# Optimization experiments

Measured on AMD Instinct MI355X. Metric: run time of the kernel, lower is better.

## Reference

```python
import jax, jax.numpy as jnp
import numpy as np

N = 50000      # nodes
E = 800000     # edges (no self loops; added in reference like PyG add_self_loops)
IN = 128       # in_channel
C = 64         # out_channel
K = 64         # cos_num (correlation embedding dim)
H = 1          # heads
NEG_SLOPE = 0.2


def setup_inputs() -> dict:
    key = jax.random.key(0)
    ks = jax.random.split(key, 10)
    x = jax.random.normal(ks[0], (N, IN), dtype=jnp.float32)
    corrs = jax.random.normal(ks[1], (N, K), dtype=jnp.float32)
    # random edges guaranteed to have src != dst (original remove_self_loops)
    src = jax.random.randint(ks[2], (E,), 0, N)
    off = jax.random.randint(ks[3], (E,), 1, N)
    dst = (src + off) % N
    edge_index = jnp.stack([src, dst]).astype(jnp.int32)  # [2, E]
    W = jax.random.normal(ks[4], (IN, H * C), dtype=jnp.float32) / np.sqrt(IN)
    att_i = jax.random.normal(ks[5], (1, H, C), dtype=jnp.float32) * 0.1
    att_j = jax.random.normal(ks[6], (1, H, C), dtype=jnp.float32) * 0.1
    att_em_i = jax.random.normal(ks[7], (1, H, K), dtype=jnp.float32) * 0.1
    att_em_j = jax.random.normal(ks[8], (1, H, K), dtype=jnp.float32) * 0.1
    bias = jnp.zeros((C,), dtype=jnp.float32)
    return {"x": x, "edge_index": edge_index, "corrs": corrs, "W": W,
            "att_i": att_i, "att_j": att_j,
            "att_em_i": att_em_i, "att_em_j": att_em_j, "bias": bias}


def reference(x, edge_index, corrs, W, att_i, att_j, att_em_i, att_em_j, bias):
    # add self loops (original: remove_self_loops then add_self_loops)
    loops = jnp.arange(N, dtype=edge_index.dtype)
    src = jnp.concatenate([edge_index[0], loops])   # [E+N] message sources (x_j)
    dst = jnp.concatenate([edge_index[1], loops])   # [E+N] message targets (x_i)

    g = (x @ W).reshape(N, H, C)                    # linear projection, [N,H,C]
    gj = g[src]                                     # source features per edge [E+N,H,C]
    gi = g[dst]                                     # target features per edge
    ej = corrs[src][:, None, :]                     # [E+N,1,K] broadcast over heads
    ei = corrs[dst][:, None, :]

    # GAT-style score on concatenated key [g || corr]
    alpha = (jnp.sum(gi * att_i, -1) + jnp.sum(ei * att_em_i, -1)
             + jnp.sum(gj * att_j, -1) + jnp.sum(ej * att_em_j, -1))   # [E+N,H]
    alpha = jax.nn.leaky_relu(alpha, NEG_SLOPE)

    # neighbor softmax over incoming edges of each target node (per head)
    amax = jax.ops.segment_max(alpha, dst, num_segments=N)
    ex = jnp.exp(alpha - amax[dst])
    denom = jax.ops.segment_sum(ex, dst, num_segments=N)
    a = ex / (denom[dst] + 1e-16)                   # [E+N,H]

    # scatter-add weighted messages
    out = jax.ops.segment_sum(gj * a[..., None], dst, num_segments=N)  # [N,H,C]
    out = out.mean(axis=1) + bias                    # concat=False -> head mean

    # wrapper: float cast + ReLU
    return jax.nn.relu(out.astype(jnp.float32))
```

## Files before the change

kernel.cpp:

```cpp
#include <hip/hip_runtime.h>
#include <hip/hip_bf16.h>
#include <math.h>

#define IN_DIM 128
#define C_DIM 64

typedef short bf16x8 __attribute__((ext_vector_type(8)));
typedef float f32x4 __attribute__((ext_vector_type(4)));

static __device__ __forceinline__ unsigned short f2bf(float f) {
    unsigned int u = __float_as_uint(f);
    u += 0x7FFFu + ((u >> 16) & 1u);
    return (unsigned short)(u >> 16);
}
static __device__ __forceinline__ float bf2f(unsigned short h) {
    return __uint_as_float(((unsigned int)h) << 16);
}

#define BKT_CHUNK 4096

__global__ __launch_bounds__(256) void k_gemm_bucket(
    const float* __restrict__ x, const float* __restrict__ W,
    const float* __restrict__ corrs,
    const float* __restrict__ att_i, const float* __restrict__ att_j,
    const float* __restrict__ att_em_i, const float* __restrict__ att_em_j,
    unsigned short* __restrict__ g_bf, float* __restrict__ s_i, float* __restrict__ s_j,
    int N, int GB,
    const int* __restrict__ src, const int* __restrict__ dst,
    int E, int NB, int CAP,
    int* __restrict__ bucket_cnt, unsigned int* __restrict__ staging)
{
    __shared__ __attribute__((aligned(16))) unsigned short WT[2][64][128];
    __shared__ int cnt[128];
    __shared__ int run[128];
    __shared__ int cur[128];

    int tid = threadIdx.x;

    if (blockIdx.x >= GB) {
        if (tid < 128) cnt[tid] = 0;
        __syncthreads();

        int T = E + N;
        int base = (blockIdx.x - GB) * BKT_CHUNK;
#pragma unroll
        for (int k = 0; k < BKT_CHUNK / 256; ++k) {
            int i = base + k * 256 + tid;
            if (i < T) {
                int d = (i < E) ? dst[i] : (i - E);
                atomicAdd(&cnt[d >> 9], 1);
            }
        }
        __syncthreads();
        if (tid < NB && cnt[tid] > 0) run[tid] = atomicAdd(&bucket_cnt[tid], cnt[tid]);
        if (tid < 128) cur[tid] = 0;
        __syncthreads();
#pragma unroll
        for (int k = 0; k < BKT_CHUNK / 256; ++k) {
            int i = base + k * 256 + tid;
            if (i < T) {
                int d, s;
                if (i < E) { d = dst[i]; s = src[i]; }
                else       { d = i - E; s = d; }
                int b = d >> 9;
                int ofs = atomicAdd(&cur[b], 1);
                int pos = run[b] + ofs;
                if (pos < CAP)
                    staging[(size_t)b * CAP + pos] =
                        (unsigned)s | ((unsigned)(d & 511) << 16);
            }
        }
        return;
    }

#pragma unroll
    for (int p = 0; p < 8; ++p) {
        int f = p * 1024 + tid * 4;
        f32x4 w4 = *(const f32x4*)(W + f);
        int k  = f >> 6;
        int c0 = f & 63;
#pragma unroll
        for (int i = 0; i < 4; ++i) {
            int c = c0 + i;
            float wv = w4[i];
            unsigned short hi = f2bf(wv);
            unsigned short lo = f2bf(wv - bf2f(hi));
            int ks = k ^ ((c & 7) << 3);
            WT[0][c][ks] = hi;
            WT[1][c][ks] = lo;
        }
    }
    __syncthreads();

    int wv = tid >> 6, lane = tid & 63;
    int mrow = lane & 15;
    int kgrp = lane >> 4;
    int row  = blockIdx.x * 64 + wv * 16 + mrow;
    int rowc = min(row, N - 1);

    f32x4 acc[4];
#pragma unroll
    for (int t = 0; t < 4; ++t) { f32x4 z = {0.f, 0.f, 0.f, 0.f}; acc[t] = z; }

    f32x4 xa[4], xb[4];
#pragma unroll
    for (int s = 0; s < 4; ++s) {
        const float* xp = x + (size_t)rowc * IN_DIM + s * 32 + kgrp * 8;
        xa[s] = *(const f32x4*)xp;
        xb[s] = *(const f32x4*)(xp + 4);
    }

#pragma unroll
    for (int s = 0; s < 4; ++s) {
        bf16x8 ah, al;
#pragma unroll
        for (int i = 0; i < 4; ++i) {
            unsigned short h0 = f2bf(xa[s][i]);
            ah[i]     = (short)h0;
            al[i]     = (short)f2bf(xa[s][i] - bf2f(h0));
            unsigned short h1 = f2bf(xb[s][i]);
            ah[4 + i] = (short)h1;
            al[4 + i] = (short)f2bf(xb[s][i] - bf2f(h1));
        }
        int kbase = s * 32 + kgrp * 8;
#pragma unroll
        for (int t = 0; t < 4; ++t) {
            int c  = t * 16 + mrow;
            int ks = kbase ^ ((c & 7) << 3);
            bf16x8 bh = *(const bf16x8*)&WT[0][c][ks];
            bf16x8 bl = *(const bf16x8*)&WT[1][c][ks];
            acc[t] = __builtin_amdgcn_mfma_f32_16x16x32_bf16(ah, bh, acc[t], 0, 0, 0);
            acc[t] = __builtin_amdgcn_mfma_f32_16x16x32_bf16(ah, bl, acc[t], 0, 0, 0);
            acc[t] = __builtin_amdgcn_mfma_f32_16x16x32_bf16(al, bh, acc[t], 0, 0, 0);
        }
    }

    float ai[4], aj[4], aei[4], aej[4];
#pragma unroll
    for (int t = 0; t < 4; ++t) {
        ai[t]  = att_i[t * 16 + mrow];
        aj[t]  = att_j[t * 16 + mrow];
        aei[t] = att_em_i[t * 16 + mrow];
        aej[t] = att_em_j[t * 16 + mrow];
    }
    int crow_base = blockIdx.x * 64 + wv * 16 + (lane >> 4) * 4;
#pragma unroll
    for (int r = 0; r < 4; ++r) {
        int grow  = crow_base + r;
        int growc = min(grow, N - 1);
        float vi = 0.f, vj = 0.f;
        ushort4 hv;
#pragma unroll
        for (int t = 0; t < 4; ++t) {
            float gv = acc[t][r];
            float cv = corrs[(size_t)growc * 64 + t * 16 + mrow];
            unsigned short h = f2bf(gv);
            if (t == 0) hv.x = h; else if (t == 1) hv.y = h;
            else if (t == 2) hv.z = h; else hv.w = h;
            vi = fmaf(gv, ai[t], fmaf(cv, aei[t], vi));
            vj = fmaf(gv, aj[t], fmaf(cv, aej[t], vj));
        }
        if (grow < N)
            *(ushort4*)(g_bf + (size_t)grow * C_DIM + mrow * 4) = hv;
#pragma unroll
        for (int o = 1; o < 16; o <<= 1) {
            vi += __shfl_xor(vi, o);
            vj += __shfl_xor(vj, o);
        }
        if (mrow == 0 && grow < N) { s_i[grow] = vi; s_j[grow] = vj; }
    }
}

__global__ __launch_bounds__(256) void k_scatter(
    const unsigned int* __restrict__ staging, const int* __restrict__ bucket_cnt,
    int N, int CAP,
    const float* __restrict__ s_i, const float* __restrict__ s_j,
    int* __restrict__ row_start, int* __restrict__ row_end,
    unsigned int* __restrict__ edge_rec)
{
    __shared__ int cnt[512];
    __shared__ int off[513];
    __shared__ int cur[512];
    __shared__ int wsum[4];
    __shared__ float si_l[512];

    int b = blockIdx.x, t = threadIdx.x;
    int lo = b << 9;
    int hi = min(lo + 512, N);
    int bcnt = min(bucket_cnt[b], CAP);
    const unsigned int* sb = staging + (size_t)b * CAP;

    cnt[2 * t] = 0; cnt[2 * t + 1] = 0;
    if (lo + 2 * t     < N) si_l[2 * t]     = s_i[lo + 2 * t];
    if (lo + 2 * t + 1 < N) si_l[2 * t + 1] = s_i[lo + 2 * t + 1];
    __syncthreads();

    for (int r = t; r < bcnt; r += 256)
        atomicAdd(&cnt[(sb[r] >> 16) & 511], 1);
    __syncthreads();

    int a0 = cnt[2 * t], a1 = cnt[2 * t + 1];
    int s = a0 + a1;
    int lane = t & 63, wv = t >> 6;
    int incl = s;
#pragma unroll
    for (int o = 1; o < 64; o <<= 1) {
        int u = __shfl_up(incl, o);
        if (lane >= o) incl += u;
    }
    if (lane == 63) wsum[wv] = incl;
    __syncthreads();
    int woff = 0;
    for (int w = 0; w < wv; ++w) woff += wsum[w];
    int ex = woff + incl - s;
    off[2 * t] = ex;       off[2 * t + 1] = ex + a0;
    cur[2 * t] = ex;       cur[2 * t + 1] = ex + a0;
    if (t == 255) off[512] = woff + incl;
    __syncthreads();

    int rawb = b * CAP;
    for (int i = t; i < hi - lo; i += 256) {
        row_start[lo + i] = rawb + off[i];
        row_end[lo + i]   = rawb + off[i + 1];
    }
    for (int r = t; r < bcnt; r += 256) {
        unsigned int rec = sb[r];
        int dl   = (rec >> 16) & 511;
        int srcn = rec & 0xFFFFu;
        float a = si_l[dl] + s_j[srcn];
        a = (a > 0.f) ? a : 0.2f * a;
        float w = __expf(a);
        int slot = atomicAdd(&cur[dl], 1);
        edge_rec[rawb + slot] = ((unsigned)f2bf(w) << 16) | (unsigned)srcn;
    }
}

__global__ __launch_bounds__(256) void k_aggregate(
    const unsigned short* __restrict__ g_bf,
    const int* __restrict__ row_start, const int* __restrict__ row_end,
    const unsigned int* __restrict__ edge_rec,
    const float* __restrict__ bias, float* __restrict__ out, int N)
{
    int wave = threadIdx.x >> 6, lane = threadIdx.x & 63;
    int n = blockIdx.x * 4 + wave;
    if (n >= N) return;

    int start = row_start[n];
    int end   = row_end[n];

    int grp = lane >> 3;
    int cl  = lane & 7;
    float a0 = 0.f, a1 = 0.f, a2 = 0.f, a3 = 0.f;
    float a4 = 0.f, a5 = 0.f, a6 = 0.f, a7 = 0.f, den = 0.f;
#pragma unroll 2
    for (int e0 = start; e0 < end; e0 += 8) {
        int e = e0 + grp;
        if (e < end) {
            unsigned int rec = edge_rec[e];
            int   srcn = rec & 0xFFFFu;
            float w    = bf2f((unsigned short)(rec >> 16));
            const ushort4* gp = (const ushort4*)(g_bf + (size_t)srcn * C_DIM + (cl << 3));
            ushort4 g0 = gp[0];
            ushort4 g1 = gp[1];
            a0 = fmaf(w, bf2f(g0.x), a0);
            a1 = fmaf(w, bf2f(g0.y), a1);
            a2 = fmaf(w, bf2f(g0.z), a2);
            a3 = fmaf(w, bf2f(g0.w), a3);
            a4 = fmaf(w, bf2f(g1.x), a4);
            a5 = fmaf(w, bf2f(g1.y), a5);
            a6 = fmaf(w, bf2f(g1.z), a6);
            a7 = fmaf(w, bf2f(g1.w), a7);
            den += w;
        }
    }
#pragma unroll
    for (int o = 8; o < 64; o <<= 1) {
        a0  += __shfl_xor(a0, o);
        a1  += __shfl_xor(a1, o);
        a2  += __shfl_xor(a2, o);
        a3  += __shfl_xor(a3, o);
        a4  += __shfl_xor(a4, o);
        a5  += __shfl_xor(a5, o);
        a6  += __shfl_xor(a6, o);
        a7  += __shfl_xor(a7, o);
        den += __shfl_xor(den, o);
    }
    if (grp == 0) {
        float inv = 1.f / (den + 1e-16f);
        float av[8] = {a0, a1, a2, a3, a4, a5, a6, a7};
        float* op = out + (size_t)n * C_DIM;
#pragma unroll
        for (int j = 0; j < 8; ++j) {
            int p  = (cl << 3) + j;
            int ch = ((p & 3) << 4) + (p >> 2);
            op[ch] = fmaxf(fmaf(av[j], inv, bias[ch]), 0.f);
        }
    }
}

extern "C" void kernel_launch(void* const* d_in, const int* in_sizes, int n_in,
                              void* d_out, int out_size, void* d_ws, size_t ws_size,
                              hipStream_t stream)
{
    const float* x        = (const float*)d_in[0];
    const int*   eidx     = (const int*)  d_in[1];
    const float* corrs    = (const float*)d_in[2];
    const float* W        = (const float*)d_in[3];
    const float* att_i    = (const float*)d_in[4];
    const float* att_j    = (const float*)d_in[5];
    const float* att_em_i = (const float*)d_in[6];
    const float* att_em_j = (const float*)d_in[7];
    const float* bias     = (const float*)d_in[8];
    float* out = (float*)d_out;

    int N = in_sizes[0] / IN_DIM;
    int E = in_sizes[1] / 2;
    const int* src = eidx;
    const int* dst = eidx + E;

    int T  = E + N;
    int NB = (N + 511) >> 9;
    int CAP = ((T + NB - 1) / NB);
    CAP = CAP + CAP / 4;
    CAP = (CAP + 63) & ~63;

    char* ws = (char*)d_ws;
    size_t off = 0;
    auto alloc = [&](size_t bytes) -> void* {
        void* p = ws + off;
        off += (bytes + 255) & ~(size_t)255;
        return p;
    };
    unsigned short* g_bf = (unsigned short*)alloc((size_t)N * C_DIM * sizeof(unsigned short));
    float* s_i       = (float*)alloc((size_t)N * sizeof(float));
    float* s_j       = (float*)alloc((size_t)N * sizeof(float));
    unsigned int* staging  = (unsigned int*)alloc((size_t)NB * CAP * sizeof(unsigned int));
    unsigned int* edge_rec = (unsigned int*)alloc((size_t)NB * CAP * sizeof(unsigned int));
    int*   row_start = (int*)alloc((size_t)N * sizeof(int));
    int*   row_end   = (int*)alloc((size_t)N * sizeof(int));
    int*   bucket_cnt= (int*)alloc(128 * sizeof(int));
    (void)ws_size; (void)n_in; (void)out_size;

    hipMemsetAsync(bucket_cnt, 0, 128 * sizeof(int), stream);

    int GB = (N + 63) / 64;
    int BB = (T + BKT_CHUNK - 1) / BKT_CHUNK;
    k_gemm_bucket<<<GB + BB, 256, 0, stream>>>(
        x, W, corrs, att_i, att_j, att_em_i, att_em_j, g_bf, s_i, s_j,
        N, GB, src, dst, E, NB, CAP, bucket_cnt, staging);

    k_scatter<<<NB, 256, 0, stream>>>(
        staging, bucket_cnt, N, CAP, s_i, s_j, row_start, row_end, edge_rec);

    k_aggregate<<<(N + 3) / 4, 256, 0, stream>>>(
        g_bf, row_start, row_end, edge_rec, bias, out, N);
}
```

Measured before the change: 86.29 us.

## Fuse GEMM/bucket, scatter and aggregate into one cooperative persistent kernel

Merges the three kernels into a single cooperative kernel that uses grid-wide syncs between phases, with blocks striding over virtual block indices and shared memory overlaid through a union. The goal is to remove two kernel-launch gaps and the tail effects between phases. In exchange it adds grid.sync costs and caps the grid at occupancy times 256 CUs. The scatter phase now runs on only NB (~98) blocks while the rest of the grid waits, and the occupancy query plus cooperative launch add host-side overhead.

```diff
diff --git a/kernel.cpp b/kernel.cpp
--- a/kernel.cpp
+++ b/kernel.cpp
@@ -1,9 +1,13 @@
 #include <hip/hip_runtime.h>
+#include <hip/hip_cooperative_groups.h>
 #include <hip/hip_bf16.h>
 #include <math.h>
 
+namespace cg = cooperative_groups;
+
 #define IN_DIM 128
 #define C_DIM 64
+#define BKT_CHUNK 4096
 
 typedef short bf16x8 __attribute__((ext_vector_type(8)));
 typedef float f32x4 __attribute__((ext_vector_type(4)));
@@ -17,283 +21,278 @@
     return __uint_as_float(((unsigned int)h) << 16);
 }
 
-#define BKT_CHUNK 4096
-
-__global__ __launch_bounds__(256) void k_gemm_bucket(
+struct SmemG { unsigned short WT[2][64][128]; };
+struct SmemB { int cnt[128]; int run[128]; int cur[128]; };
+struct SmemS { int cnt[512]; int off[513]; int cur[512];
+               int wsum[4]; float si_l[512]; };
+union  SmemU { SmemG g; SmemB b; SmemS s; };
+
+__global__ __launch_bounds__(256) void k_fused(
     const float* __restrict__ x, const float* __restrict__ W,
     const float* __restrict__ corrs,
     const float* __restrict__ att_i, const float* __restrict__ att_j,
     const float* __restrict__ att_em_i, const float* __restrict__ att_em_j,
     unsigned short* __restrict__ g_bf, float* __restrict__ s_i, float* __restrict__ s_j,
-    int N, int GB,
     const int* __restrict__ src, const int* __restrict__ dst,
-    int E, int NB, int CAP,
-    int* __restrict__ bucket_cnt, unsigned int* __restrict__ staging)
+    int N, int E, int GB, int BB, int NB, int CAP,
+    int* __restrict__ bucket_cnt, unsigned int* __restrict__ staging,
+    unsigned int* __restrict__ edge_rec,
+    int* __restrict__ row_start, int* __restrict__ row_end,
+    const float* __restrict__ bias, float* __restrict__ out)
 {
-    __shared__ __attribute__((aligned(16))) unsigned short WT[2][64][128];
-    __shared__ int cnt[128];
-    __shared__ int run[128];
-    __shared__ int cur[128];
-
+    __shared__ SmemU sm;
+    cg::grid_group grid = cg::this_grid();
     int tid = threadIdx.x;
-
-    if (blockIdx.x >= GB) {
-        if (tid < 128) cnt[tid] = 0;
-        __syncthreads();
-
-        int T = E + N;
-        int base = (blockIdx.x - GB) * BKT_CHUNK;
-#pragma unroll
-        for (int k = 0; k < BKT_CHUNK / 256; ++k) {
-            int i = base + k * 256 + tid;
-            if (i < T) {
-                int d = (i < E) ? dst[i] : (i - E);
-                atomicAdd(&cnt[d >> 9], 1);
-            }
-        }
-        __syncthreads();
-        if (tid < NB && cnt[tid] > 0) run[tid] = atomicAdd(&bucket_cnt[tid], cnt[tid]);
-        if (tid < 128) cur[tid] = 0;
-        __syncthreads();
-#pragma unroll
-        for (int k = 0; k < BKT_CHUNK / 256; ++k) {
-            int i = base + k * 256 + tid;
-            if (i < T) {
-                int d, s;
-                if (i < E) { d = dst[i]; s = src[i]; }
-                else       { d = i - E; s = d; }
-                int b = d >> 9;
-                int ofs = atomicAdd(&cur[b], 1);
-                int pos = run[b] + ofs;
-                if (pos < CAP)
-                    staging[(size_t)b * CAP + pos] =
-                        (unsigned)s | ((unsigned)(d & 511) << 16);
-            }
-        }
-        return;
+    int T = E + N;
+
+    for (int vb = blockIdx.x; vb < GB + BB; vb += gridDim.x) {
+        if (vb >= GB) {
+            if (tid < 128) sm.b.cnt[tid] = 0;
+            __syncthreads();
+            int base = (vb - GB) * BKT_CHUNK;
+#pragma unroll
+            for (int k = 0; k < BKT_CHUNK / 256; ++k) {
+                int i = base + k * 256 + tid;
+                if (i < T) {
+                    int d = (i < E) ? dst[i] : (i - E);
+                    atomicAdd(&sm.b.cnt[d >> 9], 1);
+                }
+            }
+            __syncthreads();
+            if (tid < NB && sm.b.cnt[tid] > 0)
+                sm.b.run[tid] = atomicAdd(&bucket_cnt[tid], sm.b.cnt[tid]);
+            if (tid < 128) sm.b.cur[tid] = 0;
+            __syncthreads();
+#pragma unroll
+            for (int k = 0; k < BKT_CHUNK / 256; ++k) {
+                int i = base + k * 256 + tid;
+                if (i < T) {
+                    int d, s;
+                    if (i < E) { d = dst[i]; s = src[i]; }
+                    else       { d = i - E; s = d; }
+                    int b = d >> 9;
+                    int ofs = atomicAdd(&sm.b.cur[b], 1);
+                    int pos = sm.b.run[b] + ofs;
+                    if (pos < CAP)
+                        staging[(size_t)b * CAP + pos] =
+                            (unsigned)s | ((unsigned)(d & 511) << 16);
+                }
+            }
+        } else {
+#pragma unroll
+            for (int p = 0; p < 8; ++p) {
+                int f = p * 1024 + tid * 4;
+                f32x4 w4 = *(const f32x4*)(W + f);
+                int k  = f >> 6;
+                int c0 = f & 63;
+#pragma unroll
+                for (int i = 0; i < 4; ++i) {
+                    int c = c0 + i;
+                    float wv2 = w4[i];
+                    unsigned short hi = f2bf(wv2);
+                    unsigned short lo = f2bf(wv2 - bf2f(hi));
+                    int ks = k ^ ((c & 7) << 3);
+                    sm.g.WT[0][c][ks] = hi;
+                    sm.g.WT[1][c][ks] = lo;
+                }
+            }
+            __syncthreads();
+
+            int wv = tid >> 6, lane = tid & 63;
+            int mrow = lane & 15;
+            int kgrp = lane >> 4;
+            int row  = vb * 64 + wv * 16 + mrow;
+            int rowc = min(row, N - 1);
+
+            f32x4 acc[4];
+#pragma unroll
+            for (int t = 0; t < 4; ++t) { f32x4 z = {0.f, 0.f, 0.f, 0.f}; acc[t] = z; }
+
+            f32x4 xa[4], xb[4];
+#pragma unroll
+            for (int s = 0; s < 4; ++s) {
+                const float* xp = x + (size_t)rowc * IN_DIM + s * 32 + kgrp * 8;
+                xa[s] = *(const f32x4*)xp;
+                xb[s] = *(const f32x4*)(xp + 4);
+            }
+
+#pragma unroll
+            for (int s = 0; s < 4; ++s) {
+                bf16x8 ah, al;
+#pragma unroll
+                for (int i = 0; i < 4; ++i) {
+                    unsigned short h0 = f2bf(xa[s][i]);
+                    ah[i]     = (short)h0;
+                    al[i]     = (short)f2bf(xa[s][i] - bf2f(h0));
+                    unsigned short h1 = f2bf(xb[s][i]);
+                    ah[4 + i] = (short)h1;
+                    al[4 + i] = (short)f2bf(xb[s][i] - bf2f(h1));
+                }
+                int kbase = s * 32 + kgrp * 8;
+#pragma unroll
+                for (int t = 0; t < 4; ++t) {
+                    int c  = t * 16 + mrow;
+                    int ks = kbase ^ ((c & 7) << 3);
+                    bf16x8 bh = *(const bf16x8*)&sm.g.WT[0][c][ks];
+                    bf16x8 bl = *(const bf16x8*)&sm.g.WT[1][c][ks];
+                    acc[t] = __builtin_amdgcn_mfma_f32_16x16x32_bf16(ah, bh, acc[t], 0, 0, 0);
+                    acc[t] = __builtin_amdgcn_mfma_f32_16x16x32_bf16(ah, bl, acc[t], 0, 0, 0);
+                    acc[t] = __builtin_amdgcn_mfma_f32_16x16x32_bf16(al, bh, acc[t], 0, 0, 0);
+                }
+            }
+
+            float ai[4], aj[4], aei[4], aej[4];
+#pragma unroll
+            for (int t = 0; t < 4; ++t) {
+                ai[t]  = att_i[t * 16 + mrow];
+                aj[t]  = att_j[t * 16 + mrow];
+                aei[t] = att_em_i[t * 16 + mrow];
+                aej[t] = att_em_j[t * 16 + mrow];
+            }
+            int crow_base = vb * 64 + wv * 16 + (lane >> 4) * 4;
+#pragma unroll
+            for (int r = 0; r < 4; ++r) {
+                int grow  = crow_base + r;
+                int growc = min(grow, N - 1);
+                float vi = 0.f, vj = 0.f;
+                ushort4 hv;
+#pragma unroll
+                for (int t = 0; t < 4; ++t) {
+                    float gv = acc[t][r];
+                    float cv = corrs[(size_t)growc * 64 + t * 16 + mrow];
+                    unsigned short h = f2bf(gv);
+                    if (t == 0) hv.x = h; else if (t == 1) hv.y = h;
+                    else if (t == 2) hv.z = h; else hv.w = h;
+                    vi = fmaf(gv, ai[t], fmaf(cv, aei[t], vi));
+                    vj = fmaf(gv, aj[t], fmaf(cv, aej[t], vj));
+                }
+                if (grow < N)
+                    *(ushort4*)(g_bf + (size_t)grow * C_DIM + mrow * 4) = hv;
+#pragma unroll
+                for (int o = 1; o < 16; o <<= 1) {
+                    vi += __shfl_xor(vi, o);
+                    vj += __shfl_xor(vj, o);
+                }
+                if (mrow == 0 && grow < N) { s_i[grow] = vi; s_j[grow] = vj; }
+            }
+        }
+        __syncthreads();
     }
 
-#pragma unroll
-    for (int p = 0; p < 8; ++p) {
-        int f = p * 1024 + tid * 4;
-        f32x4 w4 = *(const f32x4*)(W + f);
-        int k  = f >> 6;
-        int c0 = f & 63;
-#pragma unroll
-        for (int i = 0; i < 4; ++i) {
-            int c = c0 + i;
-            float wv = w4[i];
-            unsigned short hi = f2bf(wv);
-            unsigned short lo = f2bf(wv - bf2f(hi));
-            int ks = k ^ ((c & 7) << 3);
-            WT[0][c][ks] = hi;
-            WT[1][c][ks] = lo;
-        }
+    grid.sync();
+
+    for (int b = blockIdx.x; b < NB; b += gridDim.x) {
+        int t = tid;
+        int lo = b << 9;
+        int hi = min(lo + 512, N);
+        int bcnt = min(bucket_cnt[b], CAP);
+        const unsigned int* sb = staging + (size_t)b * CAP;
+
+        sm.s.cnt[2 * t] = 0; sm.s.cnt[2 * t + 1] = 0;
+        if (lo + 2 * t     < N) sm.s.si_l[2 * t]     = s_i[lo + 2 * t];
+        if (lo + 2 * t + 1 < N) sm.s.si_l[2 * t + 1] = s_i[lo + 2 * t + 1];
+        __syncthreads();
+
+        for (int r = t; r < bcnt; r += 256)
+            atomicAdd(&sm.s.cnt[(sb[r] >> 16) & 511], 1);
+        __syncthreads();
+
+        int a0 = sm.s.cnt[2 * t], a1 = sm.s.cnt[2 * t + 1];
+        int s = a0 + a1;
+        int lane = t & 63, wv = t >> 6;
+        int incl = s;
+#pragma unroll
+        for (int o = 1; o < 64; o <<= 1) {
+            int u = __shfl_up(incl, o);
+            if (lane >= o) incl += u;
+        }
+        if (lane == 63) sm.s.wsum[wv] = incl;
+        __syncthreads();
+        int woff = 0;
+        for (int w = 0; w < wv; ++w) woff += sm.s.wsum[w];
+        int ex = woff + incl - s;
+        sm.s.off[2 * t] = ex;       sm.s.off[2 * t + 1] = ex + a0;
+        sm.s.cur[2 * t] = ex;       sm.s.cur[2 * t + 1] = ex + a0;
+        if (t == 255) sm.s.off[512] = woff + incl;
+        __syncthreads();
+
+        int rawb = b * CAP;
+        for (int i = t; i < hi - lo; i += 256) {
+            row_start[lo + i] = rawb + sm.s.off[i];
+            row_end[lo + i]   = rawb + sm.s.off[i + 1];
+        }
+        for (int r = t; r < bcnt; r += 256) {
+            unsigned int rec = sb[r];
+            int dl   = (rec >> 16) & 511;
+            int srcn = rec & 0xFFFFu;
+            float a = sm.s.si_l[dl] + s_j[srcn];
+            a = (a > 0.f) ? a : 0.2f * a;
+            float w = __expf(a);
+            int slot = atomicAdd(&sm.s.cur[dl], 1);
+            edge_rec[rawb + slot] = ((unsigned)f2bf(w) << 16) | (unsigned)srcn;
+        }
+        __syncthreads();
     }
-    __syncthreads();
-
-    int wv = tid >> 6, lane = tid & 63;
-    int mrow = lane & 15;
-    int kgrp = lane >> 4;
-    int row  = blockIdx.x * 64 + wv * 16 + mrow;
-    int rowc = min(row, N - 1);
-
-    f32x4 acc[4];
-#pragma unroll
-    for (int t = 0; t < 4; ++t) { f32x4 z = {0.f, 0.f, 0.f, 0.f}; acc[t] = z; }
-
-    f32x4 xa[4], xb[4];
-#pragma unroll
-    for (int s = 0; s < 4; ++s) {
-        const float* xp = x + (size_t)rowc * IN_DIM + s * 32 + kgrp * 8;
-        xa[s] = *(const f32x4*)xp;
-        xb[s] = *(const f32x4*)(xp + 4);
-    }
-
-#pragma unroll
-    for (int s = 0; s < 4; ++s) {
-        bf16x8 ah, al;
-#pragma unroll
-        for (int i = 0; i < 4; ++i) {
-            unsigned short h0 = f2bf(xa[s][i]);
-            ah[i]     = (short)h0;
-            al[i]     = (short)f2bf(xa[s][i] - bf2f(h0));
-            unsigned short h1 = f2bf(xb[s][i]);
-            ah[4 + i] = (short)h1;
-            al[4 + i] = (short)f2bf(xb[s][i] - bf2f(h1));
-        }
-        int kbase = s * 32 + kgrp * 8;
-#pragma unroll
-        for (int t = 0; t < 4; ++t) {
-            int c  = t * 16 + mrow;
-            int ks = kbase ^ ((c & 7) << 3);
-            bf16x8 bh = *(const bf16x8*)&WT[0][c][ks];
-            bf16x8 bl = *(const bf16x8*)&WT[1][c][ks];
-            acc[t] = __builtin_amdgcn_mfma_f32_16x16x32_bf16(ah, bh, acc[t], 0, 0, 0);
-            acc[t] = __builtin_amdgcn_mfma_f32_16x16x32_bf16(ah, bl, acc[t], 0, 0, 0);
-            acc[t] = __builtin_amdgcn_mfma_f32_16x16x32_bf16(al, bh, acc[t], 0, 0, 0);
-        }
-    }
-
-    float ai[4], aj[4], aei[4], aej[4];
-#pragma unroll
-    for (int t = 0; t < 4; ++t) {
-        ai[t]  = att_i[t * 16 + mrow];
-        aj[t]  = att_j[t * 16 + mrow];
-        aei[t] = att_em_i[t * 16 + mrow];
-        aej[t] = att_em_j[t * 16 + mrow];
-    }
-    int crow_base = blockIdx.x * 64 + wv * 16 + (lane >> 4) * 4;
-#pragma unroll
-    for (int r = 0; r < 4; ++r) {
-        int grow  = crow_base + r;
-        int growc = min(grow, N - 1);
-        float vi = 0.f, vj = 0.f;
-        ushort4 hv;
-#pragma unroll
-        for (int t = 0; t < 4; ++t) {
-            float gv = acc[t][r];
-            float cv = corrs[(size_t)growc * 64 + t * 16 + mrow];
-            unsigned short h = f2bf(gv);
-            if (t == 0) hv.x = h; else if (t == 1) hv.y = h;
-            else if (t == 2) hv.z = h; else hv.w = h;
-            vi = fmaf(gv, ai[t], fmaf(cv, aei[t], vi));
-            vj = fmaf(gv, aj[t], fmaf(cv, aej[t], vj));
-        }
-        if (grow < N)
-            *(ushort4*)(g_bf + (size_t)grow * C_DIM + mrow * 4) = hv;
-#pragma unroll
-        for (int o = 1; o < 16; o <<= 1) {
-            vi += __shfl_xor(vi, o);
-            vj += __shfl_xor(vj, o);
-        }
-        if (mrow == 0 && grow < N) { s_i[grow] = vi; s_j[grow] = vj; }
-    }
-}
-
-__global__ __launch_bounds__(256) void k_scatter(
-    const unsigned int* __restrict__ staging, const int* __restrict__ bucket_cnt,
-    int N, int CAP,
-    const float* __restrict__ s_i, const float* __restrict__ s_j,
-    int* __restrict__ row_start, int* __restrict__ row_end,
-    unsigned int* __restrict__ edge_rec)
-{
-    __shared__ int cnt[512];
-    __shared__ int off[513];
-    __shared__ int cur[512];
-    __shared__ int wsum[4];
-    __shared__ float si_l[512];
-
-    int b = blockIdx.x, t = threadIdx.x;
-    int lo = b << 9;
-    int hi = min(lo + 512, N);
-    int bcnt = min(bucket_cnt[b], CAP);
-    const unsigned int* sb = staging + (size_t)b * CAP;
-
-    cnt[2 * t] = 0; cnt[2 * t + 1] = 0;
-    if (lo + 2 * t     < N) si_l[2 * t]     = s_i[lo + 2 * t];
-    if (lo + 2 * t + 1 < N) si_l[2 * t + 1] = s_i[lo + 2 * t + 1];
-    __syncthreads();
-
-    for (int r = t; r < bcnt; r += 256)
-        atomicAdd(&cnt[(sb[r] >> 16) & 511], 1);
-    __syncthreads();
-
-    int a0 = cnt[2 * t], a1 = cnt[2 * t + 1];
-    int s = a0 + a1;
-    int lane = t & 63, wv = t >> 6;
-    int incl = s;
-#pragma unroll
-    for (int o = 1; o < 64; o <<= 1) {
-        int u = __shfl_up(incl, o);
-        if (lane >= o) incl += u;
-    }
-    if (lane == 63) wsum[wv] = incl;
-    __syncthreads();
-    int woff = 0;
-    for (int w = 0; w < wv; ++w) woff += wsum[w];
-    int ex = woff + incl - s;
-    off[2 * t] = ex;       off[2 * t + 1] = ex + a0;
-    cur[2 * t] = ex;       cur[2 * t + 1] = ex + a0;
-    if (t == 255) off[512] = woff + incl;
-    __syncthreads();
-
-    int rawb = b * CAP;
-    for (int i = t; i < hi - lo; i += 256) {
-        row_start[lo + i] = rawb + off[i];
-        row_end[lo + i]   = rawb + off[i + 1];
-    }
-    for (int r = t; r < bcnt; r += 256) {
-        unsigned int rec = sb[r];
-        int dl   = (rec >> 16) & 511;
-        int srcn = rec & 0xFFFFu;
-        float a = si_l[dl] + s_j[srcn];
-        a = (a > 0.f) ? a : 0.2f * a;
-        float w = __expf(a);
-        int slot = atomicAdd(&cur[dl], 1);
-        edge_rec[rawb + slot] = ((unsigned)f2bf(w) << 16) | (unsigned)srcn;
-    }
-}
-
-__global__ __launch_bounds__(256) void k_aggregate(
-    const unsigned short* __restrict__ g_bf,
-    const int* __restrict__ row_start, const int* __restrict__ row_end,
-    const unsigned int* __restrict__ edge_rec,
-    const float* __restrict__ bias, float* __restrict__ out, int N)
-{
-    int wave = threadIdx.x >> 6, lane = threadIdx.x & 63;
-    int n = blockIdx.x * 4 + wave;
-    if (n >= N) return;
-
-    int start = row_start[n];
-    int end   = row_end[n];
-
-    int grp = lane >> 3;
-    int cl  = lane & 7;
-    float a0 = 0.f, a1 = 0.f, a2 = 0.f, a3 = 0.f;
-    float a4 = 0.f, a5 = 0.f, a6 = 0.f, a7 = 0.f, den = 0.f;
+
+    grid.sync();
+
+    {
+        int wave = tid >> 6, lane = tid & 63;
+        int grp = lane >> 3;
+        int cl  = lane & 7;
+        int nq = (N + 3) >> 2;
+        for (int q = blockIdx.x; q < nq; q += gridDim.x) {
+            int n = q * 4 + wave;
+            if (n >= N) continue;
+            int start = row_start[n];
+            int end   = row_end[n];
+
+            float a0 = 0.f, a1 = 0.f, a2 = 0.f, a3 = 0.f;
+            float a4 = 0.f, a5 = 0.f, a6 = 0.f, a7 = 0.f, den = 0.f;
 #pragma unroll 2
-    for (int e0 = start; e0 < end; e0 += 8) {
-        int e = e0 + grp;
-        if (e < end) {
-            unsigned int rec = edge_rec[e];
-            int   srcn = rec & 0xFFFFu;
-            float w    = bf2f((unsigned short)(rec >> 16));
-            const ushort4* gp = (const ushort4*)(g_bf + (size_t)srcn * C_DIM + (cl << 3));
-            ushort4 g0 = gp[0];
-            ushort4 g1 = gp[1];
-            a0 = fmaf(w, bf2f(g0.x), a0);
-            a1 = fmaf(w, bf2f(g0.y), a1);
-            a2 = fmaf(w, bf2f(g0.z), a2);
-            a3 = fmaf(w, bf2f(g0.w), a3);
-            a4 = fmaf(w, bf2f(g1.x), a4);
-            a5 = fmaf(w, bf2f(g1.y), a5);
-            a6 = fmaf(w, bf2f(g1.z), a6);
-            a7 = fmaf(w, bf2f(g1.w), a7);
-            den += w;
-        }
-    }
-#pragma unroll
-    for (int o = 8; o < 64; o <<= 1) {
-        a0  += __shfl_xor(a0, o);
-        a1  += __shfl_xor(a1, o);
-        a2  += __shfl_xor(a2, o);
-        a3  += __shfl_xor(a3, o);
-        a4  += __shfl_xor(a4, o);
-        a5  += __shfl_xor(a5, o);
-        a6  += __shfl_xor(a6, o);
-        a7  += __shfl_xor(a7, o);
-        den += __shfl_xor(den, o);
-    }
-    if (grp == 0) {
-        float inv = 1.f / (den + 1e-16f);
-        float av[8] = {a0, a1, a2, a3, a4, a5, a6, a7};
-        float* op = out + (size_t)n * C_DIM;
-#pragma unroll
-        for (int j = 0; j < 8; ++j) {
-            int p  = (cl << 3) + j;
-            int ch = ((p & 3) << 4) + (p >> 2);
-            op[ch] = fmaxf(fmaf(av[j], inv, bias[ch]), 0.f);
+            for (int e0 = start; e0 < end; e0 += 8) {
+                int e = e0 + grp;
+                if (e < end) {
+                    unsigned int rec = edge_rec[e];
+                    int   srcn = rec & 0xFFFFu;
+                    float w    = bf2f((unsigned short)(rec >> 16));
+                    const ushort4* gp = (const ushort4*)(g_bf + (size_t)srcn * C_DIM + (cl << 3));
+                    ushort4 g0 = gp[0];
+                    ushort4 g1 = gp[1];
+                    a0 = fmaf(w, bf2f(g0.x), a0);
+                    a1 = fmaf(w, bf2f(g0.y), a1);
+                    a2 = fmaf(w, bf2f(g0.z), a2);
+                    a3 = fmaf(w, bf2f(g0.w), a3);
+                    a4 = fmaf(w, bf2f(g1.x), a4);
+                    a5 = fmaf(w, bf2f(g1.y), a5);
+                    a6 = fmaf(w, bf2f(g1.z), a6);
+                    a7 = fmaf(w, bf2f(g1.w), a7);
+                    den += w;
+                }
+            }
+#pragma unroll
+            for (int o = 8; o < 64; o <<= 1) {
+                a0  += __shfl_xor(a0, o);
+                a1  += __shfl_xor(a1, o);
+                a2  += __shfl_xor(a2, o);
+                a3  += __shfl_xor(a3, o);
+                a4  += __shfl_xor(a4, o);
+                a5  += __shfl_xor(a5, o);
+                a6  += __shfl_xor(a6, o);
+                a7  += __shfl_xor(a7, o);
+                den += __shfl_xor(den, o);
+            }
+            if (grp == 0) {
+                float inv = 1.f / (den + 1e-16f);
+                float av[8] = {a0, a1, a2, a3, a4, a5, a6, a7};
+                float* op = out + (size_t)n * C_DIM;
+#pragma unroll
+                for (int j = 0; j < 8; ++j) {
+                    int p  = (cl << 3) + j;
+                    int ch = ((p & 3) << 4) + (p >> 2);
+                    op[ch] = fmaxf(fmaf(av[j], inv, bias[ch]), 0.f);
+                }
+            }
         }
     }
 }
@@ -345,13 +344,24 @@
 
     int GB = (N + 63) / 64;
     int BB = (T + BKT_CHUNK - 1) / BKT_CHUNK;
-    k_gemm_bucket<<<GB + BB, 256, 0, stream>>>(
-        x, W, corrs, att_i, att_j, att_em_i, att_em_j, g_bf, s_i, s_j,
-        N, GB, src, dst, E, NB, CAP, bucket_cnt, staging);
-
-    k_scatter<<<NB, 256, 0, stream>>>(
-        staging, bucket_cnt, N, CAP, s_i, s_j, row_start, row_end, edge_rec);
-
-    k_aggregate<<<(N + 3) / 4, 256, 0, stream>>>(
-        g_bf, row_start, row_end, edge_rec, bias, out, N);
+
+    int occ = 0;
+    hipOccupancyMaxActiveBlocksPerMultiprocessor(&occ, k_fused, 256, 0);
+    if (occ < 1) occ = 1;
+    int maxco = occ * 256;
+    int need  = GB + BB;
+    int gridn = need < maxco ? need : maxco;
+
+    void* args[] = {
+        (void*)&x, (void*)&W, (void*)&corrs,
+        (void*)&att_i, (void*)&att_j, (void*)&att_em_i, (void*)&att_em_j,
+        (void*)&g_bf, (void*)&s_i, (void*)&s_j,
+        (void*)&src, (void*)&dst,
+        (void*)&N, (void*)&E, (void*)&GB, (void*)&BB, (void*)&NB, (void*)&CAP,
+        (void*)&bucket_cnt, (void*)&staging, (void*)&edge_rec,
+        (void*)&row_start, (void*)&row_end,
+        (void*)&bias, (void*)&out
+    };
+    hipLaunchCooperativeKernel((void*)k_fused, dim3(gridn), dim3(256),
+                               args, 0, stream);
 }
```

Measured after the change: 260.7 us. 202% more time.
